# Optimization experiments

Measured on AMD Instinct MI355X. Metric: run time of the kernel, lower is better.

Reference implementation:

```python
import jax, jax.numpy as jnp
import numpy as np

BETA = 0.05
KNN = 6
N_SPLITS = 10


def setup_inputs() -> dict:
    key = jax.random.key(0)
    k1, k2, k3 = jax.random.split(key, 3)
    B, C, F = 256, 32768, 2048
    inputs = jax.random.normal(k1, (B, F), dtype=jnp.float32)
    inputs = inputs / jnp.linalg.norm(inputs, axis=1, keepdims=True)  # re-ID features are L2-normalized
    em = jax.random.normal(k2, (C, F), dtype=jnp.float32)
    em = em / jnp.linalg.norm(em, axis=1, keepdims=True)  # memory rows kept unit-norm by EMA update
    targets = jax.random.randint(k3, (B,), 0, C, dtype=jnp.int64)
    return {"inputs": inputs, "em": em, "targets": targets, "epoch": 10}


def reference(inputs, em, targets, epoch):
    B, Fdim = inputs.shape
    C = em.shape[0]
    step = -(-Fdim // N_SPLITS)  # ceil, matches step+=1 logic in torch

    # full similarity against memory bank: [B, C]
    sim = (inputs @ em.T) / BETA

    # per-feature-split similarities: [n_splits, B, C]
    sims = jnp.stack([
        (inputs[:, step * i: min(step * (i + 1), Fdim)]
         @ em[:, step * i: min(step * (i + 1), Fdim)].T) / BETA
        for i in range(N_SPLITS)
    ])

    logp = jax.nn.log_softmax(sim, axis=1)  # [B, C]

    if KNN > 0 and epoch > 4:
        # top-k neighbors per split (descending sort -> first k)
        _, topk = jax.lax.top_k(sims, KNN)  # [n_splits, B, KNN]
        s_idx = jnp.arange(N_SPLITS)[:, None, None]
        b_idx = jnp.arange(B)[None, :, None]
        # scatter uniform weight 1/k at knn indices, then force 1.0 at the true target
        onehot = jnp.zeros((N_SPLITS, B, C), dtype=sim.dtype)
        onehot = onehot.at[s_idx, b_idx, topk].set(1.0 / KNN)
        onehot = onehot.at[jnp.arange(N_SPLITS)[:, None],
                           jnp.arange(B)[None, :],
                           targets[None, :]].set(1.0)
        # mean over splits of mean_b sum_c -(t * log p)
        loss = (-(onehot * logp[None, :, :]).sum(axis=2)).mean(axis=1).mean()
    else:
        loss = -jnp.take_along_axis(logp, targets[:, None], axis=1).mean()
    return loss
```

## Files before the change

### kernel.cpp

```cpp
#include <hip/hip_runtime.h>
#include <stdint.h>


typedef float f32x4 __attribute__((ext_vector_type(4)));
typedef __bf16 bf16x8 __attribute__((ext_vector_type(8)));
typedef unsigned short u16x8 __attribute__((ext_vector_type(8)));

#define NB 256
#define NC 32768
#define NF 2048
#define NSPLIT 10
#define SPLITW 205
#define BN 128
#define NBLK (NC / BN)
#define PAD 48
#define INV_BETA 20.0f

__device__ __forceinline__ unsigned short f2bf(float f) {
  uint32_t u = __float_as_uint(f);
  return (unsigned short)((u + 0x7FFFu + ((u >> 16) & 1u)) >> 16);
}

__device__ __forceinline__ bf16x8 asbf(u16x8 v) {
  union { u16x8 u; bf16x8 b; } x; x.u = v; return x.b;
}

__global__ void k_zero(float* __restrict__ sumexp, float* __restrict__ out) {
  int t = threadIdx.x;
  if (t < NB) sumexp[t] = 0.f;
  if (t == 0) out[0] = 0.f;
}

__global__ __launch_bounds__(512, 2)
void k_main(const float* __restrict__ inp, const float* __restrict__ em,
            float* __restrict__ sim, unsigned long long* __restrict__ cand,
            float* __restrict__ sumexp) {
  __shared__ unsigned short Alds[NB * PAD];
  __shared__ unsigned short Blds[BN * PAD];

  const int t  = threadIdx.x;
  const int l  = t & 63;
  const int w  = t >> 6;
  const int li = l & 15;
  const int lg = l >> 4;
  const int bx = blockIdx.x;
  const int c0 = bx * BN;

  const f32x4 Z4 = {0.f, 0.f, 0.f, 0.f};
  f32x4 accT[2][8], accS[2][8];
  #pragma unroll
  for (int m = 0; m < 2; m++)
    #pragma unroll
    for (int n = 0; n < 8; n++) { accT[m][n] = Z4; accS[m][n] = Z4; }

  auto finalize = [&](int s) {
    #pragma unroll
    for (int m = 0; m < 2; m++)
      #pragma unroll
      for (int n = 0; n < 8; n++) accT[m][n] += accS[m][n];
    #pragma unroll
    for (int m = 0; m < 2; m++) {
      #pragma unroll
      for (int j = 0; j < 4; j++) {
        uint32_t p[8];
        #pragma unroll
        for (int n = 0; n < 8; n++) {
          uint32_t u = __float_as_uint(accS[m][n][j]);
          u ^= (uint32_t)(((int32_t)u) >> 31) | 0x80000000u;
          p[n] = (u & 0xFFFFFF80u) | (uint32_t)(n * 16 + li);
        }
        uint32_t res[6];
        #pragma unroll
        for (int r = 0; r < 6; r++) {
          uint32_t mx = p[0];
          #pragma unroll
          for (int n = 1; n < 8; n++) mx = mx > p[n] ? mx : p[n];
          #pragma unroll
          for (int d = 1; d < 16; d <<= 1) {
            uint32_t o = __shfl_xor(mx, d);
            mx = mx > o ? mx : o;
          }
          res[r] = mx;
          #pragma unroll
          for (int n = 0; n < 8; n++) p[n] = (p[n] == mx) ? 0u : p[n];
        }
        if (li == 0) {
          int rowg = w * 32 + m * 16 + lg * 4 + j;
          unsigned long long* dst = cand + (((size_t)s * NB + rowg) * NBLK + bx) * 6;
          #pragma unroll
          for (int r = 0; r < 6; r++) {
            uint32_t colg = (uint32_t)c0 + (res[r] & 127u);
            dst[r] = ((unsigned long long)(res[r] & 0xFFFFFF80u) << 32)
                   | (unsigned long long)(0xFFFFu ^ colg);
          }
        }
      }
    }
    #pragma unroll
    for (int m = 0; m < 2; m++)
      #pragma unroll
      for (int n = 0; n < 8; n++) accS[m][n] = Z4;
  };

  for (int kk = 0; kk < 64; ++kk) {
    const int k0 = kk * 32;
    __syncthreads();
    #pragma unroll
    for (int i = 0; i < 4; i++) {
      int id = t + i * 512, ar = id >> 3, kv = id & 7;
      float4 v = *(const float4*)(inp + (size_t)ar * NF + k0 + kv * 4);
      ushort4 h; h.x = f2bf(v.x); h.y = f2bf(v.y); h.z = f2bf(v.z); h.w = f2bf(v.w);
      *(ushort4*)(&Alds[ar * PAD + kv * 4]) = h;
    }
    #pragma unroll
    for (int i = 0; i < 2; i++) {
      int id = t + i * 512, br = id >> 3, kv = id & 7;
      float4 v = *(const float4*)(em + (size_t)(c0 + br) * NF + k0 + kv * 4);
      ushort4 h; h.x = f2bf(v.x); h.y = f2bf(v.y); h.z = f2bf(v.z); h.w = f2bf(v.w);
      *(ushort4*)(&Blds[br * PAD + kv * 4]) = h;
    }
    __syncthreads();

    u16x8 af[2], bfv[8];
    #pragma unroll
    for (int m = 0; m < 2; m++)
      af[m] = *(const u16x8*)(&Alds[(w * 32 + m * 16 + li) * PAD + lg * 8]);
    #pragma unroll
    for (int n = 0; n < 8; n++)
      bfv[n] = *(const u16x8*)(&Blds[(n * 16 + li) * PAD + lg * 8]);

    const int s0 = k0 / SPLITW;
    const int s1 = (k0 + 31) / SPLITW;
    if (s1 > s0) {
      const int thr = s1 * SPLITW - k0;
      u16x8 alo[2], ahi[2];
      #pragma unroll
      for (int m = 0; m < 2; m++) {
        #pragma unroll
        for (int e = 0; e < 8; e++) {
          bool in_lo = (lg * 8 + e) < thr;
          alo[m][e] = in_lo ? af[m][e] : (unsigned short)0;
          ahi[m][e] = in_lo ? (unsigned short)0 : af[m][e];
        }
      }
      #pragma unroll
      for (int m = 0; m < 2; m++)
        #pragma unroll
        for (int n = 0; n < 8; n++)
          accS[m][n] = __builtin_amdgcn_mfma_f32_16x16x32_bf16(
              asbf(alo[m]), asbf(bfv[n]), accS[m][n], 0, 0, 0);
      finalize(s0);
      #pragma unroll
      for (int m = 0; m < 2; m++)
        #pragma unroll
        for (int n = 0; n < 8; n++)
          accS[m][n] = __builtin_amdgcn_mfma_f32_16x16x32_bf16(
              asbf(ahi[m]), asbf(bfv[n]), accS[m][n], 0, 0, 0);
    } else {
      #pragma unroll
      for (int m = 0; m < 2; m++)
        #pragma unroll
        for (int n = 0; n < 8; n++)
          accS[m][n] = __builtin_amdgcn_mfma_f32_16x16x32_bf16(
              asbf(af[m]), asbf(bfv[n]), accS[m][n], 0, 0, 0);
    }
  }
  finalize(NSPLIT - 1);

  #pragma unroll
  for (int m = 0; m < 2; m++) {
    #pragma unroll
    for (int j = 0; j < 4; j++) {
      int rowg = w * 32 + m * 16 + lg * 4 + j;
      float se = 0.f;
      #pragma unroll
      for (int n = 0; n < 8; n++) {
        float v = accT[m][n][j] * INV_BETA;
        sim[(size_t)rowg * NC + c0 + n * 16 + li] = v;
        se += __expf(v);
      }
      #pragma unroll
      for (int d = 1; d < 16; d <<= 1) se += __shfl_xor(se, d);
      if (li == 0) atomicAdd(&sumexp[rowg], se);
    }
  }
}

__device__ __forceinline__ void casd(unsigned long long& a, unsigned long long& b) {
  unsigned long long mx = a > b ? a : b;
  unsigned long long mn = a > b ? b : a;
  a = mx; b = mn;
}

__global__ void k_merge(const unsigned long long* __restrict__ cand,
                        const float* __restrict__ sim,
                        const float* __restrict__ sumexp,
                        const int* __restrict__ tgt,
                        float* __restrict__ out) {
  const int s = blockIdx.x >> 8;
  const int b = blockIdx.x & 255;
  const int l = threadIdx.x;

  unsigned long long t8[8];
  #pragma unroll
  for (int i = 0; i < 8; i++) t8[i] = 0ull;

  const unsigned long long* src = cand + ((size_t)s * NB + b) * (NBLK * 6);
  for (int i = 0; i < 24; i++) {
    unsigned long long v = src[l + i * 64];
    #pragma unroll
    for (int k = 0; k < 8; k++) {
      if (v > t8[k]) { unsigned long long tmp = t8[k]; t8[k] = v; v = tmp; }
    }
  }
  #pragma unroll
  for (int d = 1; d < 64; d <<= 1) {
    unsigned long long o[8], hi[8];
    #pragma unroll
    for (int i = 0; i < 8; i++) o[i] = __shfl_xor(t8[i], d);
    #pragma unroll
    for (int i = 0; i < 8; i++) {
      unsigned long long a = t8[i], bb = o[7 - i];
      hi[i] = a > bb ? a : bb;
    }
    casd(hi[0], hi[4]); casd(hi[1], hi[5]); casd(hi[2], hi[6]); casd(hi[3], hi[7]);
    casd(hi[0], hi[2]); casd(hi[1], hi[3]); casd(hi[4], hi[6]); casd(hi[5], hi[7]);
    casd(hi[0], hi[1]); casd(hi[2], hi[3]); casd(hi[4], hi[5]); casd(hi[6], hi[7]);
    #pragma unroll
    for (int i = 0; i < 8; i++) t8[i] = hi[i];
  }
  if (l == 0) {
    const int tg = tgt[b];
    const float lz = logf(sumexp[b]);
    float acc = 0.f; int cnt = 0;
    #pragma unroll
    for (int r = 0; r < 6; r++) {
      int col = (int)(((unsigned)(t8[r] & 0xFFFFull)) ^ 0xFFFFu);
      if (col != tg) { acc += sim[(size_t)b * NC + col]; cnt++; }
    }
    const float simt = sim[(size_t)b * NC + tg];
    const float contrib = (simt - lz) + (acc - (float)cnt * lz) * (1.0f / 6.0f);
    atomicAdd(out, -contrib * (1.0f / (NSPLIT * NB)));
  }
}

extern "C" void kernel_launch(void* const* d_in, const int* in_sizes, int n_in,
                              void* d_out, int out_size, void* d_ws, size_t ws_size,
                              hipStream_t stream) {
  const float* inp = (const float*)d_in[0];
  const float* em  = (const float*)d_in[1];
  const int*   tgt = (const int*)d_in[2];
  float* out = (float*)d_out;

  char* ws = (char*)d_ws;
  float* sim = (float*)ws;
  unsigned long long* cand =
      (unsigned long long*)(ws + (size_t)NB * NC * 4);
  float* sumexp = (float*)(ws + (size_t)NB * NC * 4 +
                           (size_t)NSPLIT * NB * NBLK * 6 * 8);

  k_zero<<<1, 256, 0, stream>>>(sumexp, out);
  k_main<<<NBLK, 512, 0, stream>>>(inp, em, sim, cand, sumexp);
  k_merge<<<NSPLIT * NB, 64, 0, stream>>>(cand, sim, sumexp, tgt, out);
}
```

Baseline: 784.6 us.

## Double-buffer LDS with async global-to-LDS loads, smaller tiles, compact candidates

Reworks the main GEMM loop into a double-buffered pipeline. The input tile is fetched with global_load_lds straight into XOR-swizzled LDS as fp32 and converted to bf16 when read, while the next memory-bank tile is prefetched into registers during the current MFMAs. The column tile shrinks from 128 to 64 and occupancy is raised to 4 blocks, which doubles the number of blocks and the redundant A loads. Top-k candidates are now stored as 32-bit values that the merge kernel rebuilds into 64-bit keys, halving candidate traffic, and the merge uses two independent insertion chains.

```diff
diff --git a/kernel.cpp b/kernel.cpp
--- a/kernel.cpp
+++ b/kernel.cpp
@@ -11,60 +11,78 @@
 #define NF 2048
 #define NSPLIT 10
 #define SPLITW 205
-#define BN 128
+#define BN 64
 #define NBLK (NC / BN)
-#define PAD 48
+#define NKSTEP 64
 #define INV_BETA 20.0f
 
 __device__ __forceinline__ unsigned short f2bf(float f) {
   uint32_t u = __float_as_uint(f);
   return (unsigned short)((u + 0x7FFFu + ((u >> 16) & 1u)) >> 16);
 }
-
 __device__ __forceinline__ bf16x8 asbf(u16x8 v) {
   union { u16x8 u; bf16x8 b; } x; x.u = v; return x.b;
 }
 
-__global__ void k_zero(float* __restrict__ sumexp, float* __restrict__ out) {
+#define GLDS16(g, p) __builtin_amdgcn_global_load_lds(                         \
+    (const __attribute__((address_space(1))) unsigned int*)(g),                \
+    (__attribute__((address_space(3))) unsigned int*)(p), 16, 0, 0)
+
+__global__ __launch_bounds__(256)
+void k_zero(float* __restrict__ sumexp, float* __restrict__ out) {
   int t = threadIdx.x;
   if (t < NB) sumexp[t] = 0.f;
   if (t == 0) out[0] = 0.f;
 }
 
-__global__ __launch_bounds__(512, 2)
+__global__ __launch_bounds__(512, 4)
 void k_main(const float* __restrict__ inp, const float* __restrict__ em,
-            float* __restrict__ sim, unsigned long long* __restrict__ cand,
+            float* __restrict__ sim, uint32_t* __restrict__ cand,
             float* __restrict__ sumexp) {
-  __shared__ unsigned short Alds[NB * PAD];
-  __shared__ unsigned short Blds[BN * PAD];
+  __shared__ float Af[2][8192];
+  __shared__ unsigned short Bh[2][2048];
 
   const int t  = threadIdx.x;
   const int l  = t & 63;
   const int w  = t >> 6;
-  const int li = l & 15;
-  const int lg = l >> 4;
+  const int li = l & 15, lg = l >> 4;
   const int bx = blockIdx.x;
   const int c0 = bx * BN;
 
+  const int arr = l >> 3;
+  const int ag  = (l & 7) ^ arr;
+  const int br  = t >> 3, bg = t & 7;
+  const int bus = (bg >> 1) ^ ((br >> 1) & 3);
+  const int bh2 = bg & 1;
+
   const f32x4 Z4 = {0.f, 0.f, 0.f, 0.f};
-  f32x4 accT[2][8], accS[2][8];
+  f32x4 accT[2][4], accS[2][4];
   #pragma unroll
   for (int m = 0; m < 2; m++)
     #pragma unroll
-    for (int n = 0; n < 8; n++) { accT[m][n] = Z4; accS[m][n] = Z4; }
+    for (int n = 0; n < 4; n++) { accT[m][n] = Z4; accS[m][n] = Z4; }
+
+  auto issueA = [&](int bb, int tt) {
+    #pragma unroll
+    for (int j = 0; j < 4; j++) {
+      const int c = w * 4 + j;
+      const float* g = inp + (size_t)(c * 8 + arr) * NF + tt * 32 + ag * 4;
+      GLDS16(g, &Af[bb][c * 256]);
+    }
+  };
 
   auto finalize = [&](int s) {
     #pragma unroll
     for (int m = 0; m < 2; m++)
       #pragma unroll
-      for (int n = 0; n < 8; n++) accT[m][n] += accS[m][n];
+      for (int n = 0; n < 4; n++) accT[m][n] += accS[m][n];
     #pragma unroll
     for (int m = 0; m < 2; m++) {
       #pragma unroll
       for (int j = 0; j < 4; j++) {
-        uint32_t p[8];
-        #pragma unroll
-        for (int n = 0; n < 8; n++) {
+        uint32_t p[4];
+        #pragma unroll
+        for (int n = 0; n < 4; n++) {
           uint32_t u = __float_as_uint(accS[m][n][j]);
           u ^= (uint32_t)(((int32_t)u) >> 31) | 0x80000000u;
           p[n] = (u & 0xFFFFFF80u) | (uint32_t)(n * 16 + li);
@@ -74,7 +92,7 @@
         for (int r = 0; r < 6; r++) {
           uint32_t mx = p[0];
           #pragma unroll
-          for (int n = 1; n < 8; n++) mx = mx > p[n] ? mx : p[n];
+          for (int n = 1; n < 4; n++) mx = mx > p[n] ? mx : p[n];
           #pragma unroll
           for (int d = 1; d < 16; d <<= 1) {
             uint32_t o = __shfl_xor(mx, d);
@@ -82,99 +100,110 @@
           }
           res[r] = mx;
           #pragma unroll
-          for (int n = 0; n < 8; n++) p[n] = (p[n] == mx) ? 0u : p[n];
+          for (int n = 0; n < 4; n++) p[n] = (p[n] == mx) ? 0u : p[n];
         }
         if (li == 0) {
-          int rowg = w * 32 + m * 16 + lg * 4 + j;
-          unsigned long long* dst = cand + (((size_t)s * NB + rowg) * NBLK + bx) * 6;
+          const int rowg = w * 32 + m * 16 + lg * 4 + j;
+          uint32_t* dst = cand + ((size_t)(s * NB + rowg) * NBLK + bx) * 6;
           #pragma unroll
-          for (int r = 0; r < 6; r++) {
-            uint32_t colg = (uint32_t)c0 + (res[r] & 127u);
-            dst[r] = ((unsigned long long)(res[r] & 0xFFFFFF80u) << 32)
-                   | (unsigned long long)(0xFFFFu ^ colg);
-          }
+          for (int r = 0; r < 6; r++) dst[r] = res[r];
         }
       }
-    }
-    #pragma unroll
-    for (int m = 0; m < 2; m++)
-      #pragma unroll
-      for (int n = 0; n < 8; n++) accS[m][n] = Z4;
+      #pragma unroll
+      for (int n = 0; n < 4; n++) accS[m][n] = Z4;
+    }
   };
 
-  for (int kk = 0; kk < 64; ++kk) {
-    const int k0 = kk * 32;
-    __syncthreads();
-    #pragma unroll
-    for (int i = 0; i < 4; i++) {
-      int id = t + i * 512, ar = id >> 3, kv = id & 7;
-      float4 v = *(const float4*)(inp + (size_t)ar * NF + k0 + kv * 4);
-      ushort4 h; h.x = f2bf(v.x); h.y = f2bf(v.y); h.z = f2bf(v.z); h.w = f2bf(v.w);
-      *(ushort4*)(&Alds[ar * PAD + kv * 4]) = h;
-    }
-    #pragma unroll
-    for (int i = 0; i < 2; i++) {
-      int id = t + i * 512, br = id >> 3, kv = id & 7;
-      float4 v = *(const float4*)(em + (size_t)(c0 + br) * NF + k0 + kv * 4);
-      ushort4 h; h.x = f2bf(v.x); h.y = f2bf(v.y); h.z = f2bf(v.z); h.w = f2bf(v.w);
-      *(ushort4*)(&Blds[br * PAD + kv * 4]) = h;
-    }
-    __syncthreads();
-
-    u16x8 af[2], bfv[8];
-    #pragma unroll
-    for (int m = 0; m < 2; m++)
-      af[m] = *(const u16x8*)(&Alds[(w * 32 + m * 16 + li) * PAD + lg * 8]);
-    #pragma unroll
-    for (int n = 0; n < 8; n++)
-      bfv[n] = *(const u16x8*)(&Blds[(n * 16 + li) * PAD + lg * 8]);
-
-    const int s0 = k0 / SPLITW;
-    const int s1 = (k0 + 31) / SPLITW;
+  auto step = [&](int tt, int cb, int nb) {
+    f32x4 bv;
+    const bool pre = (tt + 1 < NKSTEP);
+    if (pre) {
+      issueA(nb, tt + 1);
+      bv = *(const f32x4*)(em + (size_t)(c0 + br) * NF + (tt + 1) * 32 + bg * 4);
+    }
+    u16x8 af[2];
+    #pragma unroll
+    for (int m = 0; m < 2; m++) {
+      const int chunk = w * 4 + m * 2 + (li >> 3);
+      const int rr = li & 7;
+      const float* bp = &Af[cb][chunk * 256 + rr * 32];
+      f32x4 x0 = *(const f32x4*)(bp + (((lg << 1)    ) ^ rr) * 4);
+      f32x4 x1 = *(const f32x4*)(bp + (((lg << 1) | 1) ^ rr) * 4);
+      u16x8 r;
+      r[0] = f2bf(x0[0]); r[1] = f2bf(x0[1]); r[2] = f2bf(x0[2]); r[3] = f2bf(x0[3]);
+      r[4] = f2bf(x1[0]); r[5] = f2bf(x1[1]); r[6] = f2bf(x1[2]); r[7] = f2bf(x1[3]);
+      af[m] = r;
+    }
+    u16x8 bfv[4];
+    #pragma unroll
+    for (int n = 0; n < 4; n++) {
+      const int rowp = n * 16 + li;
+      const int sl = lg ^ ((rowp >> 1) & 3);
+      bfv[n] = *(const u16x8*)&Bh[cb][rowp * 32 + sl * 8];
+    }
+    const int k0 = tt * 32;
+    const int s0 = k0 / SPLITW, s1 = (k0 + 31) / SPLITW;
     if (s1 > s0) {
       const int thr = s1 * SPLITW - k0;
-      u16x8 alo[2], ahi[2];
-      #pragma unroll
-      for (int m = 0; m < 2; m++) {
-        #pragma unroll
-        for (int e = 0; e < 8; e++) {
-          bool in_lo = (lg * 8 + e) < thr;
-          alo[m][e] = in_lo ? af[m][e] : (unsigned short)0;
-          ahi[m][e] = in_lo ? (unsigned short)0 : af[m][e];
-        }
-      }
-      #pragma unroll
-      for (int m = 0; m < 2; m++)
-        #pragma unroll
-        for (int n = 0; n < 8; n++)
+      u16x8 am[2];
+      #pragma unroll
+      for (int m = 0; m < 2; m++)
+        #pragma unroll
+        for (int e = 0; e < 8; e++)
+          am[m][e] = (lg * 8 + e) < thr ? af[m][e] : (unsigned short)0;
+      #pragma unroll
+      for (int m = 0; m < 2; m++)
+        #pragma unroll
+        for (int n = 0; n < 4; n++)
           accS[m][n] = __builtin_amdgcn_mfma_f32_16x16x32_bf16(
-              asbf(alo[m]), asbf(bfv[n]), accS[m][n], 0, 0, 0);
+              asbf(am[m]), asbf(bfv[n]), accS[m][n], 0, 0, 0);
       finalize(s0);
       #pragma unroll
       for (int m = 0; m < 2; m++)
         #pragma unroll
-        for (int n = 0; n < 8; n++)
+        for (int e = 0; e < 8; e++)
+          am[m][e] = (lg * 8 + e) < thr ? (unsigned short)0 : af[m][e];
+      #pragma unroll
+      for (int m = 0; m < 2; m++)
+        #pragma unroll
+        for (int n = 0; n < 4; n++)
           accS[m][n] = __builtin_amdgcn_mfma_f32_16x16x32_bf16(
-              asbf(ahi[m]), asbf(bfv[n]), accS[m][n], 0, 0, 0);
+              asbf(am[m]), asbf(bfv[n]), accS[m][n], 0, 0, 0);
     } else {
       #pragma unroll
       for (int m = 0; m < 2; m++)
         #pragma unroll
-        for (int n = 0; n < 8; n++)
+        for (int n = 0; n < 4; n++)
           accS[m][n] = __builtin_amdgcn_mfma_f32_16x16x32_bf16(
               asbf(af[m]), asbf(bfv[n]), accS[m][n], 0, 0, 0);
     }
-  }
+    if (pre) {
+      ushort4 hh;
+      hh.x = f2bf(bv[0]); hh.y = f2bf(bv[1]); hh.z = f2bf(bv[2]); hh.w = f2bf(bv[3]);
+      *(ushort4*)&Bh[nb][br * 32 + bus * 8 + bh2 * 4] = hh;
+    }
+    __syncthreads();
+  };
+
+  {
+    issueA(0, 0);
+    f32x4 bv = *(const f32x4*)(em + (size_t)(c0 + br) * NF + bg * 4);
+    ushort4 hh;
+    hh.x = f2bf(bv[0]); hh.y = f2bf(bv[1]); hh.z = f2bf(bv[2]); hh.w = f2bf(bv[3]);
+    *(ushort4*)&Bh[0][br * 32 + bus * 8 + bh2 * 4] = hh;
+    __syncthreads();
+  }
+  for (int tt = 0; tt < NKSTEP; tt += 2) { step(tt, 0, 1); step(tt + 1, 1, 0); }
   finalize(NSPLIT - 1);
 
   #pragma unroll
   for (int m = 0; m < 2; m++) {
     #pragma unroll
     for (int j = 0; j < 4; j++) {
-      int rowg = w * 32 + m * 16 + lg * 4 + j;
+      const int rowg = w * 32 + m * 16 + lg * 4 + j;
       float se = 0.f;
       #pragma unroll
-      for (int n = 0; n < 8; n++) {
+      for (int n = 0; n < 4; n++) {
         float v = accT[m][n][j] * INV_BETA;
         sim[(size_t)rowg * NC + c0 + n * 16 + li] = v;
         se += __expf(v);
@@ -192,42 +221,58 @@
   a = mx; b = mn;
 }
 
-__global__ void k_merge(const unsigned long long* __restrict__ cand,
-                        const float* __restrict__ sim,
-                        const float* __restrict__ sumexp,
-                        const int* __restrict__ tgt,
-                        float* __restrict__ out) {
+__device__ __forceinline__ void merge8(unsigned long long* a,
+                                       const unsigned long long* b) {
+  unsigned long long hi[8];
+  #pragma unroll
+  for (int i = 0; i < 8; i++) {
+    unsigned long long x = a[i], y = b[7 - i];
+    hi[i] = x > y ? x : y;
+  }
+  casd(hi[0], hi[4]); casd(hi[1], hi[5]); casd(hi[2], hi[6]); casd(hi[3], hi[7]);
+  casd(hi[0], hi[2]); casd(hi[1], hi[3]); casd(hi[4], hi[6]); casd(hi[5], hi[7]);
+  casd(hi[0], hi[1]); casd(hi[2], hi[3]); casd(hi[4], hi[5]); casd(hi[6], hi[7]);
+  #pragma unroll
+  for (int i = 0; i < 8; i++) a[i] = hi[i];
+}
+
+__global__ __launch_bounds__(64)
+void k_merge(const uint32_t* __restrict__ cand, const float* __restrict__ sim,
+             const float* __restrict__ sumexp, const int* __restrict__ tgt,
+             float* __restrict__ out) {
   const int s = blockIdx.x >> 8;
   const int b = blockIdx.x & 255;
   const int l = threadIdx.x;
 
-  unsigned long long t8[8];
-  #pragma unroll
-  for (int i = 0; i < 8; i++) t8[i] = 0ull;
-
-  const unsigned long long* src = cand + ((size_t)s * NB + b) * (NBLK * 6);
-  for (int i = 0; i < 24; i++) {
-    unsigned long long v = src[l + i * 64];
+  const uint32_t* src = cand + (size_t)(s * NB + b) * (NBLK * 6);
+  unsigned long long ta[8], tb[8];
+  #pragma unroll
+  for (int i = 0; i < 8; i++) { ta[i] = 0ull; tb[i] = 0ull; }
+
+  #pragma unroll 6
+  for (int i = 0; i < 48; i += 2) {
+    const int i0 = l + i * 64, i1 = l + (i + 1) * 64;
+    const uint32_t e0 = src[i0], e1 = src[i1];
+    const uint32_t c0g = (uint32_t)(i0 / 6) * 64u + (e0 & 63u);
+    const uint32_t c1g = (uint32_t)(i1 / 6) * 64u + (e1 & 63u);
+    unsigned long long v0 = ((unsigned long long)(e0 & 0xFFFFFF80u) << 32)
+                          | (unsigned long long)(0xFFFFu ^ c0g);
+    unsigned long long v1 = ((unsigned long long)(e1 & 0xFFFFFF80u) << 32)
+                          | (unsigned long long)(0xFFFFu ^ c1g);
     #pragma unroll
     for (int k = 0; k < 8; k++) {
-      if (v > t8[k]) { unsigned long long tmp = t8[k]; t8[k] = v; v = tmp; }
-    }
-  }
+      if (v0 > ta[k]) { unsigned long long tmp = ta[k]; ta[k] = v0; v0 = tmp; }
+      if (v1 > tb[k]) { unsigned long long tmp = tb[k]; tb[k] = v1; v1 = tmp; }
+    }
+  }
+  merge8(ta, tb);
+
   #pragma unroll
   for (int d = 1; d < 64; d <<= 1) {
-    unsigned long long o[8], hi[8];
-    #pragma unroll
-    for (int i = 0; i < 8; i++) o[i] = __shfl_xor(t8[i], d);
-    #pragma unroll
-    for (int i = 0; i < 8; i++) {
-      unsigned long long a = t8[i], bb = o[7 - i];
-      hi[i] = a > bb ? a : bb;
-    }
-    casd(hi[0], hi[4]); casd(hi[1], hi[5]); casd(hi[2], hi[6]); casd(hi[3], hi[7]);
-    casd(hi[0], hi[2]); casd(hi[1], hi[3]); casd(hi[4], hi[6]); casd(hi[5], hi[7]);
-    casd(hi[0], hi[1]); casd(hi[2], hi[3]); casd(hi[4], hi[5]); casd(hi[6], hi[7]);
-    #pragma unroll
-    for (int i = 0; i < 8; i++) t8[i] = hi[i];
+    unsigned long long o[8];
+    #pragma unroll
+    for (int i = 0; i < 8; i++) o[i] = __shfl_xor(ta[i], d);
+    merge8(ta, o);
   }
   if (l == 0) {
     const int tg = tgt[b];
@@ -235,7 +280,7 @@
     float acc = 0.f; int cnt = 0;
     #pragma unroll
     for (int r = 0; r < 6; r++) {
-      int col = (int)(((unsigned)(t8[r] & 0xFFFFull)) ^ 0xFFFFu);
+      const int col = (int)(((unsigned)(ta[r] & 0xFFFFull)) ^ 0xFFFFu);
       if (col != tg) { acc += sim[(size_t)b * NC + col]; cnt++; }
     }
     const float simt = sim[(size_t)b * NC + tg];
@@ -254,10 +299,9 @@
 
   char* ws = (char*)d_ws;
   float* sim = (float*)ws;
-  unsigned long long* cand =
-      (unsigned long long*)(ws + (size_t)NB * NC * 4);
+  uint32_t* cand = (uint32_t*)(ws + (size_t)NB * NC * 4);
   float* sumexp = (float*)(ws + (size_t)NB * NC * 4 +
-                           (size_t)NSPLIT * NB * NBLK * 6 * 8);
+                           (size_t)NSPLIT * NB * NBLK * 6 * 4);
 
   k_zero<<<1, 256, 0, stream>>>(sumexp, out);
   k_main<<<NBLK, 512, 0, stream>>>(inp, em, sim, cand, sumexp);
```

Measured after the change: 1.609 ms. 2.05x slower.
